# Kernel optimization log

Hardware: AMD Instinct MI355X
Metric: run time of the kernel (lower is better)

## Reference

```python
import jax, jax.numpy as jnp
import numpy as np

B, S, D, C = 8, 4096, 512, 2048


def setup_inputs() -> dict:
    key = jax.random.key(0)
    kx, kc = jax.random.split(key)
    x = jax.random.normal(kx, (B, S, D), dtype=jnp.float32)
    # kaiming_uniform_(a=sqrt(5)) on a [*,D,C] tensor ~ U(-bound, bound); exact init
    # distribution is irrelevant for the math, so plain scaled uniform is used.
    bound = 1.0 / np.sqrt(D)
    codebook = jax.random.uniform(kc, (1, 1, D, C), dtype=jnp.float32,
                                  minval=-bound, maxval=bound)
    return {"x": x, "codebook": codebook}


def reference(x, codebook):
    # Original: ((x[..., :, None] - codebook) ** 2).mean(dim=-2) -> [B, S, C]
    # Equivalent GEMM form: mean_d(x_d^2) + mean_d(c_dk^2) - (2/D) * x . c_k
    d = x.shape[-1]
    cb = codebook.reshape(codebook.shape[-2], codebook.shape[-1])  # [D, C]
    x2 = jnp.mean(x * x, axis=-1, keepdims=True)                   # [B, S, 1]
    c2 = jnp.mean(cb * cb, axis=0)                                 # [C]
    xc = jnp.einsum('bsd,dc->bsc', x, cb) / d                      # [B, S, C]
    return x2 + c2 - 2.0 * xc
```

## Files before the change

### kernel.cpp

```cpp
#include <hip/hip_runtime.h>
#include <hip/hip_bf16.h>


typedef __attribute__((ext_vector_type(8))) short bf16x8;
typedef __attribute__((ext_vector_type(4))) float f32x4;

#define M_ROWS 32768
#define K_DIM  512
#define N_COLS 2048

__device__ __forceinline__ unsigned short f2bf(float f) {
    unsigned int u = __float_as_uint(f);
    return (unsigned short)((u + 0x7fffu + ((u >> 16) & 1u)) >> 16);
}

__device__ __forceinline__ void gload_lds16(const void* g, void* l) {
    __builtin_amdgcn_global_load_lds(
        (const __attribute__((address_space(1))) unsigned int*)g,
        (__attribute__((address_space(3))) unsigned int*)l,
        16, 0, 0);
}

__global__ __launch_bounds__(256) void prep_x_kernel(const float* __restrict__ x,
                                                     unsigned short* __restrict__ xb,
                                                     float* __restrict__ x2) {
    const int wid = threadIdx.x >> 6;
    const int lane = threadIdx.x & 63;
    const int row = (blockIdx.x << 2) + wid;
    const float4* p4 = reinterpret_cast<const float4*>(x + (size_t)row * K_DIM);
    float4 v0 = p4[lane];
    float4 v1 = p4[lane + 64];
    float ss = v0.x*v0.x + v0.y*v0.y + v0.z*v0.z + v0.w*v0.w
             + v1.x*v1.x + v1.y*v1.y + v1.z*v1.z + v1.w*v1.w;
    union { unsigned short us[4]; uint2 u2; } pa, pb;
    pa.us[0] = f2bf(v0.x); pa.us[1] = f2bf(v0.y); pa.us[2] = f2bf(v0.z); pa.us[3] = f2bf(v0.w);
    pb.us[0] = f2bf(v1.x); pb.us[1] = f2bf(v1.y); pb.us[2] = f2bf(v1.z); pb.us[3] = f2bf(v1.w);
    uint2* dst = reinterpret_cast<uint2*>(xb + (size_t)row * K_DIM);
    dst[lane]      = pa.u2;
    dst[lane + 64] = pb.u2;
    #pragma unroll
    for (int off = 32; off; off >>= 1) ss += __shfl_xor(ss, off);
    if (lane == 0) x2[row] = ss * (1.0f / (float)K_DIM);
}

__global__ __launch_bounds__(256) void prep_cb_kernel(const float* __restrict__ cb,
                                                      unsigned short* __restrict__ cbT) {
    __shared__ float tile[32][65];
    const int k0 = blockIdx.x * 32;
    const int n0 = blockIdx.y * 64;
    const int tx = threadIdx.x & 63;
    const int ty = threadIdx.x >> 6;
    #pragma unroll
    for (int i = 0; i < 8; ++i) {
        const int k = ty + i * 4;
        tile[k][tx] = cb[(size_t)(k0 + k) * N_COLS + n0 + tx];
    }
    __syncthreads();
    const int kc = threadIdx.x & 31;
    const int nr = threadIdx.x >> 5;
    #pragma unroll
    for (int i = 0; i < 8; ++i) {
        const int n = nr + i * 8;
        cbT[(size_t)(n0 + n) * K_DIM + k0 + kc] = f2bf(tile[kc][n] * 0.00390625f);
    }
}

__global__ __launch_bounds__(256) void c2_kernel(const float* __restrict__ cb,
                                                 float* __restrict__ c2) {
    __shared__ float p[4][64];
    const int t = threadIdx.x;
    const int nl = t & 63;
    const int kc = t >> 6;
    const int n = blockIdx.x * 64 + nl;
    float s = 0.0f;
    for (int k = kc * 128; k < kc * 128 + 128; ++k) {
        float v = cb[(size_t)k * N_COLS + n];
        s += v * v;
    }
    p[kc][nl] = s;
    __syncthreads();
    if (t < 64) {
        c2[blockIdx.x * 64 + t] =
            (p[0][t] + p[1][t] + p[2][t] + p[3][t]) * (1.0f / (float)K_DIM);
    }
}

__global__ __launch_bounds__(256) void gemm_kernel(
        const unsigned short* __restrict__ A,
        const unsigned short* __restrict__ Bt,
        const float* __restrict__ x2,
        const float* __restrict__ c2,
        float* __restrict__ out) {
    __shared__ unsigned short As[128 * 32];
    __shared__ unsigned short Bs[128 * 32];
    const int tid  = threadIdx.x;
    const int wid  = tid >> 6;
    const int lane = tid & 63;
    const int wr = wid >> 1, wc = wid & 1;
    const int n0 = blockIdx.x * 128;
    const int m0 = blockIdx.y * 128;
    const int l15 = lane & 15;
    const int lhi = lane >> 4;

    f32x4 acc[4][4] = {};

    const unsigned short* Abase = A  + (size_t)m0 * K_DIM;
    const unsigned short* Bbase = Bt + (size_t)n0 * K_DIM;

    for (int k0 = 0; k0 < K_DIM; k0 += 32) {
        #pragma unroll
        for (int r = 0; r < 2; ++r) {
            const int ch  = r * 256 + tid;
            const int row = ch >> 2;
            const int ko  = (ch & 3) * 8;
            gload_lds16(Abase + (size_t)row * K_DIM + k0 + ko,
                        &As[(r * 256 + wid * 64) * 8]);
            gload_lds16(Bbase + (size_t)row * K_DIM + k0 + ko,
                        &Bs[(r * 256 + wid * 64) * 8]);
        }
        __syncthreads();

        bf16x8 aF[4], bF[4];
        #pragma unroll
        for (int i = 0; i < 4; ++i) {
            aF[i] = *reinterpret_cast<const bf16x8*>(&As[(wr * 64 + i * 16 + l15) * 32 + lhi * 8]);
            bF[i] = *reinterpret_cast<const bf16x8*>(&Bs[(wc * 64 + i * 16 + l15) * 32 + lhi * 8]);
        }
        #pragma unroll
        for (int i = 0; i < 4; ++i)
            #pragma unroll
            for (int j = 0; j < 4; ++j)
                acc[i][j] = __builtin_amdgcn_mfma_f32_16x16x32_bf16(aF[i], bF[j], acc[i][j], 0, 0, 0);
        __syncthreads();
    }

    #pragma unroll
    for (int i = 0; i < 4; ++i) {
        const int mrow = m0 + wr * 64 + i * 16 + lhi * 4;
        const float xv0 = x2[mrow + 0];
        const float xv1 = x2[mrow + 1];
        const float xv2 = x2[mrow + 2];
        const float xv3 = x2[mrow + 3];
        #pragma unroll
        for (int j = 0; j < 4; ++j) {
            const int n = n0 + wc * 64 + j * 16 + l15;
            const float cv = c2[n];
            float* o = out + (size_t)mrow * N_COLS + n;
            o[0 * N_COLS] = xv0 + cv - acc[i][j][0];
            o[1 * N_COLS] = xv1 + cv - acc[i][j][1];
            o[2 * N_COLS] = xv2 + cv - acc[i][j][2];
            o[3 * N_COLS] = xv3 + cv - acc[i][j][3];
        }
    }
}

extern "C" void kernel_launch(void* const* d_in, const int* in_sizes, int n_in,
                              void* d_out, int out_size, void* d_ws, size_t ws_size,
                              hipStream_t stream) {
    const float* x  = (const float*)d_in[0];
    const float* cb = (const float*)d_in[1];
    float* out = (float*)d_out;

    char* ws = (char*)d_ws;
    unsigned short* xb  = (unsigned short*)ws;
    unsigned short* cbT = (unsigned short*)(ws + (size_t)33554432);
    float* x2 = (float*)(ws + (size_t)33554432 + 2097152);
    float* c2 = (float*)(ws + (size_t)33554432 + 2097152 + 131072);

    prep_x_kernel<<<M_ROWS / 4, 256, 0, stream>>>(x, xb, x2);
    prep_cb_kernel<<<dim3(16, 32), 256, 0, stream>>>(cb, cbT);
    c2_kernel<<<N_COLS / 64, 256, 0, stream>>>(cb, c2);
    gemm_kernel<<<dim3(N_COLS / 128, M_ROWS / 128), 256, 0, stream>>>(xb, cbT, x2, c2, out);
}
```

Measured before the change: 151.9 us.

## Rewrite GEMM with 256x256 tiles, double-buffered swizzled LDS and XCD-aware block mapping

The GEMM now uses 512-thread blocks computing 256x256 output tiles with a K step of 64 split into half-tiles. Global-to-LDS loads are double-buffered and interleaved with MFMA phases using explicit vmcnt waits, raw barriers and s_setprio. LDS layout is XOR-swizzled to avoid bank conflicts, and the block index is remapped to group tiles per XCD for L2 reuse. This is meant to hide memory latency and raise MFMA utilization, at the cost of higher register and LDS pressure (128 KB LDS per block) and fragile manual synchronization.

Result: faster. 130.7 us (-13.9%).

```diff
diff --git a/kernel.cpp b/kernel.cpp
--- a/kernel.cpp
+++ b/kernel.cpp
@@ -8,6 +8,7 @@
 #define M_ROWS 32768
 #define K_DIM  512
 #define N_COLS 2048
+#define NT     8
 
 __device__ __forceinline__ unsigned short f2bf(float f) {
     unsigned int u = __float_as_uint(f);
@@ -85,71 +86,147 @@
     }
 }
 
-__global__ __launch_bounds__(256) void gemm_kernel(
+
+__device__ __forceinline__ void stage_half(const unsigned short* __restrict__ gbase,
+                                           unsigned short* lbase, int wid, int lane) {
+    #pragma unroll
+    for (int i = 0; i < 2; ++i) {
+        const int o16 = i * 512 + wid * 64 + lane;
+        const int row = o16 >> 2;
+        const int sl  = (o16 & 3) ^ ((row >> 1) & 3);
+        gload_lds16(gbase + (size_t)row * K_DIM + sl * 8,
+                    lbase + i * 4096 + wid * 512);
+    }
+}
+
+__device__ __forceinline__ bf16x8 frag_ld(const unsigned short* h, int r, int lhi) {
+    const int off = r * 32 + ((lhi ^ ((r >> 1) & 3)) << 3);
+    return *reinterpret_cast<const bf16x8*>(&h[off]);
+}
+
+#define BAR()  do { asm volatile("" ::: "memory"); \
+                    __builtin_amdgcn_s_barrier();  \
+                    asm volatile("" ::: "memory"); } while (0)
+
+__global__ __launch_bounds__(512, 2) void gemm_kernel(
         const unsigned short* __restrict__ A,
         const unsigned short* __restrict__ Bt,
         const float* __restrict__ x2,
         const float* __restrict__ c2,
         float* __restrict__ out) {
-    __shared__ unsigned short As[128 * 32];
-    __shared__ unsigned short Bs[128 * 32];
+    __shared__ unsigned short smem[2][4][256 * 32];
+
     const int tid  = threadIdx.x;
     const int wid  = tid >> 6;
     const int lane = tid & 63;
-    const int wr = wid >> 1, wc = wid & 1;
-    const int n0 = blockIdx.x * 128;
-    const int m0 = blockIdx.y * 128;
+    const int wr = wid >> 2;
+    const int wc = wid & 3;
     const int l15 = lane & 15;
     const int lhi = lane >> 4;
 
-    f32x4 acc[4][4] = {};
-
-    const unsigned short* Abase = A  + (size_t)m0 * K_DIM;
-    const unsigned short* Bbase = Bt + (size_t)n0 * K_DIM;
-
-    for (int k0 = 0; k0 < K_DIM; k0 += 32) {
-        #pragma unroll
-        for (int r = 0; r < 2; ++r) {
-            const int ch  = r * 256 + tid;
-            const int row = ch >> 2;
-            const int ko  = (ch & 3) * 8;
-            gload_lds16(Abase + (size_t)row * K_DIM + k0 + ko,
-                        &As[(r * 256 + wid * 64) * 8]);
-            gload_lds16(Bbase + (size_t)row * K_DIM + k0 + ko,
-                        &Bs[(r * 256 + wid * 64) * 8]);
-        }
-        __syncthreads();
-
-        bf16x8 aF[4], bF[4];
-        #pragma unroll
-        for (int i = 0; i < 4; ++i) {
-            aF[i] = *reinterpret_cast<const bf16x8*>(&As[(wr * 64 + i * 16 + l15) * 32 + lhi * 8]);
-            bF[i] = *reinterpret_cast<const bf16x8*>(&Bs[(wc * 64 + i * 16 + l15) * 32 + lhi * 8]);
-        }
-        #pragma unroll
-        for (int i = 0; i < 4; ++i)
-            #pragma unroll
-            for (int j = 0; j < 4; ++j)
-                acc[i][j] = __builtin_amdgcn_mfma_f32_16x16x32_bf16(aF[i], bF[j], acc[i][j], 0, 0, 0);
-        __syncthreads();
-    }
-
-    #pragma unroll
-    for (int i = 0; i < 4; ++i) {
-        const int mrow = m0 + wr * 64 + i * 16 + lhi * 4;
+    const int bid  = blockIdx.x;
+    const int lbid = (bid & 7) * 128 + (bid >> 3);
+    const int m0 = (lbid >> 3) * 256;
+    const int n0 = (lbid & 7) * 256;
+
+    const unsigned short* Ab = A  + (size_t)m0 * K_DIM;
+    const unsigned short* Bb = Bt + (size_t)n0 * K_DIM;
+
+    f32x4 acc[8][4] = {};
+
+    stage_half(Ab,      smem[0][0], wid, lane);
+    stage_half(Bb,      smem[0][2], wid, lane);
+    stage_half(Ab + 32, smem[0][1], wid, lane);
+    stage_half(Bb + 32, smem[0][3], wid, lane);
+    asm volatile("s_waitcnt vmcnt(4)" ::: "memory");
+    BAR();
+
+    for (int t = 0; t < NT; ++t) {
+        const int cur = t & 1, nxt = cur ^ 1;
+        const unsigned short* hA0 = smem[cur][0];
+        const unsigned short* hA1 = smem[cur][1];
+        const unsigned short* hB0 = smem[cur][2];
+        const unsigned short* hB1 = smem[cur][3];
+        const int kn = (t + 1) * 64;
+        const bool st = (t < NT - 1);
+        bf16x8 a[4], b[4];
+
+        if (st) stage_half(Ab + kn, smem[nxt][0], wid, lane);
+        #pragma unroll
+        for (int mf = 0; mf < 4; ++mf) a[mf] = frag_ld(hA0, wr * 128 + mf * 16 + l15, lhi);
+        #pragma unroll
+        for (int nf = 0; nf < 4; ++nf) b[nf] = frag_ld(hB0, wc * 64 + nf * 16 + l15, lhi);
+        BAR();
+        __builtin_amdgcn_s_setprio(1);
+        #pragma unroll
+        for (int mf = 0; mf < 4; ++mf)
+            #pragma unroll
+            for (int nf = 0; nf < 4; ++nf)
+                acc[mf][nf] = __builtin_amdgcn_mfma_f32_16x16x32_bf16(a[mf], b[nf], acc[mf][nf], 0, 0, 0);
+        __builtin_amdgcn_s_setprio(0);
+        BAR();
+
+        if (st) stage_half(Bb + kn, smem[nxt][2], wid, lane);
+        #pragma unroll
+        for (int mf = 0; mf < 4; ++mf) a[mf] = frag_ld(hA0, wr * 128 + (mf + 4) * 16 + l15, lhi);
+        BAR();
+        __builtin_amdgcn_s_setprio(1);
+        #pragma unroll
+        for (int mf = 0; mf < 4; ++mf)
+            #pragma unroll
+            for (int nf = 0; nf < 4; ++nf)
+                acc[mf + 4][nf] = __builtin_amdgcn_mfma_f32_16x16x32_bf16(a[mf], b[nf], acc[mf + 4][nf], 0, 0, 0);
+        __builtin_amdgcn_s_setprio(0);
+        if (st) asm volatile("s_waitcnt vmcnt(4)" ::: "memory");
+        else    asm volatile("s_waitcnt vmcnt(0)" ::: "memory");
+        BAR();
+
+        if (st) stage_half(Ab + kn + 32, smem[nxt][1], wid, lane);
+        #pragma unroll
+        for (int mf = 0; mf < 4; ++mf) a[mf] = frag_ld(hA1, wr * 128 + mf * 16 + l15, lhi);
+        #pragma unroll
+        for (int nf = 0; nf < 4; ++nf) b[nf] = frag_ld(hB1, wc * 64 + nf * 16 + l15, lhi);
+        BAR();
+        __builtin_amdgcn_s_setprio(1);
+        #pragma unroll
+        for (int mf = 0; mf < 4; ++mf)
+            #pragma unroll
+            for (int nf = 0; nf < 4; ++nf)
+                acc[mf][nf] = __builtin_amdgcn_mfma_f32_16x16x32_bf16(a[mf], b[nf], acc[mf][nf], 0, 0, 0);
+        __builtin_amdgcn_s_setprio(0);
+        BAR();
+
+        if (st) stage_half(Bb + kn + 32, smem[nxt][3], wid, lane);
+        #pragma unroll
+        for (int mf = 0; mf < 4; ++mf) a[mf] = frag_ld(hA1, wr * 128 + (mf + 4) * 16 + l15, lhi);
+        BAR();
+        __builtin_amdgcn_s_setprio(1);
+        #pragma unroll
+        for (int mf = 0; mf < 4; ++mf)
+            #pragma unroll
+            for (int nf = 0; nf < 4; ++nf)
+                acc[mf + 4][nf] = __builtin_amdgcn_mfma_f32_16x16x32_bf16(a[mf], b[nf], acc[mf + 4][nf], 0, 0, 0);
+        __builtin_amdgcn_s_setprio(0);
+        if (st) asm volatile("s_waitcnt vmcnt(4)" ::: "memory");
+        BAR();
+    }
+
+    #pragma unroll
+    for (int mf = 0; mf < 8; ++mf) {
+        const int mrow = m0 + wr * 128 + mf * 16 + lhi * 4;
         const float xv0 = x2[mrow + 0];
         const float xv1 = x2[mrow + 1];
         const float xv2 = x2[mrow + 2];
         const float xv3 = x2[mrow + 3];
         #pragma unroll
-        for (int j = 0; j < 4; ++j) {
-            const int n = n0 + wc * 64 + j * 16 + l15;
-            const float cv = c2[n];
-            float* o = out + (size_t)mrow * N_COLS + n;
-            o[0 * N_COLS] = xv0 + cv - acc[i][j][0];
-            o[1 * N_COLS] = xv1 + cv - acc[i][j][1];
-            o[2 * N_COLS] = xv2 + cv - acc[i][j][2];
-            o[3 * N_COLS] = xv3 + cv - acc[i][j][3];
+        for (int nf = 0; nf < 4; ++nf) {
+            const int col = n0 + wc * 64 + nf * 16 + l15;
+            const float cv = c2[col];
+            float* o = out + (size_t)mrow * N_COLS + col;
+            o[0 * N_COLS] = xv0 + cv - acc[mf][nf][0];
+            o[1 * N_COLS] = xv1 + cv - acc[mf][nf][1];
+            o[2 * N_COLS] = xv2 + cv - acc[mf][nf][2];
+            o[3 * N_COLS] = xv3 + cv - acc[mf][nf][3];
         }
     }
 }
@@ -170,5 +247,5 @@
     prep_x_kernel<<<M_ROWS / 4, 256, 0, stream>>>(x, xb, x2);
     prep_cb_kernel<<<dim3(16, 32), 256, 0, stream>>>(cb, cbT);
     c2_kernel<<<N_COLS / 64, 256, 0, stream>>>(cb, c2);
-    gemm_kernel<<<dim3(N_COLS / 128, M_ROWS / 128), 256, 0, stream>>>(xb, cbT, x2, c2, out);
-}
+    gemm_kernel<<<dim3((M_ROWS / 256) * (N_COLS / 256)), 512, 0, stream>>>(xb, cbT, x2, c2, out);
+}
```

## Rewrite GEMM as persistent double-buffered kernel overlapping epilogue stores with MFMA

Applied to the files above, without the earlier changes.

The GEMM becomes a persistent kernel with 256 blocks of 512 threads. Each block owns 256 rows and sweeps 8 column tiles of 128 over half of N. Shared-memory tiles are double-buffered and XOR-swizzled, and loads are gated with explicit vmcnt waits and barriers. The previous tile's accumulators are stored while the current tile's MFMAs run, which hides output write traffic behind compute. The cost is complex hand-scheduled macros, a risk of races in the waitcnt gating, and higher register pressure from two accumulator sets.

After: 207.3 us. 1.36x slower.

```diff
diff --git a/kernel.cpp b/kernel.cpp
--- a/kernel.cpp
+++ b/kernel.cpp
@@ -85,73 +85,197 @@
     }
 }
 
-__global__ __launch_bounds__(256) void gemm_kernel(
+#define A0OFF 0
+#define A1OFF 8192
+#define B0OFF 16384
+#define B1OFF 20480
+
+__device__ __forceinline__ void stage_halfA(const unsigned short* __restrict__ g,
+                                            unsigned short* l, int wid, int lane) {
+    #pragma unroll
+    for (int i = 0; i < 2; ++i) {
+        const int o16 = i * 512 + wid * 64 + lane;
+        const int row = o16 >> 2;
+        const int sl  = (o16 & 3) ^ ((row >> 1) & 3);
+        gload_lds16(g + (size_t)row * K_DIM + sl * 8, l + i * 4096 + wid * 512);
+    }
+}
+__device__ __forceinline__ void stage_halfB(const unsigned short* __restrict__ g,
+                                            unsigned short* l, int wid, int lane) {
+    const int o16 = wid * 64 + lane;
+    const int row = o16 >> 2;
+    const int sl  = (o16 & 3) ^ ((row >> 1) & 3);
+    gload_lds16(g + (size_t)row * K_DIM + sl * 8, l + wid * 512);
+}
+
+__device__ __forceinline__ bf16x8 frag_ld(const unsigned short* h, int r, int lhi) {
+    const int off = r * 32 + ((lhi ^ ((r >> 1) & 3)) << 3);
+    return *reinterpret_cast<const bf16x8*>(&h[off]);
+}
+
+#define BAR()  do { asm volatile("" ::: "memory"); \
+                    __builtin_amdgcn_s_barrier();  \
+                    asm volatile("" ::: "memory"); } while (0)
+#define GATE_(n) asm volatile("s_waitcnt vmcnt(" #n ")" ::: "memory")
+#define GATE(n) GATE_(n)
+
+#define STORE1(OACC, IDX)                                                      \
+  { const int i_ = (IDX);                                                      \
+    const int mf_ = i_ >> 4, nf_ = (i_ >> 2) & 3, jj_ = i_ & 3;                \
+    outOld[(size_t)(mf_ * 16 + jj_) * N_COLS + nf_ * 16] =                     \
+        x2v[mf_ * 4 + jj_] + c2o[nf_] - OACC[mf_][nf_][jj_]; }
+
+#define MFMA8(ACCC, BASE)                                                      \
+  _Pragma("unroll")                                                            \
+  for (int nf_ = 0; nf_ < 4; ++nf_) {                                          \
+    ACCC[(BASE)][nf_]     = __builtin_amdgcn_mfma_f32_16x16x32_bf16(a[(BASE)],     b[nf_], ACCC[(BASE)][nf_],     0, 0, 0); \
+    ACCC[(BASE) + 1][nf_] = __builtin_amdgcn_mfma_f32_16x16x32_bf16(a[(BASE) + 1], b[nf_], ACCC[(BASE) + 1][nf_], 0, 0, 0); \
+  }
+
+#define KTILE(KT, ACCC, ACCO, DOST, G1N, G2N, DOG2, GA, GB, DOSTG)             \
+  {                                                                            \
+    const unsigned short* hA0_ = &smem[(KT) & 1][A0OFF];                       \
+    const unsigned short* hA1_ = &smem[(KT) & 1][A1OFF];                       \
+    const unsigned short* hB0_ = &smem[(KT) & 1][B0OFF];                       \
+    const unsigned short* hB1_ = &smem[(KT) & 1][B1OFF];                       \
+    unsigned short* nxt_ = smem[((KT) + 1) & 1];                               \
+                                                                  \
+    if (DOSTG) stage_halfA(GA, nxt_ + A0OFF, wid, lane);                       \
+    a[0] = frag_ld(hA0_, wr64 +  0 + l15, lhi);                                \
+    a[1] = frag_ld(hA0_, wr64 + 16 + l15, lhi);                                \
+    _Pragma("unroll")                                                          \
+    for (int nf_ = 0; nf_ < 4; ++nf_)                                          \
+        b[nf_] = frag_ld(hB0_, wc64 + nf_ * 16 + l15, lhi);                    \
+    BAR();                                                                     \
+    __builtin_amdgcn_s_setprio(1);                                             \
+    MFMA8(ACCC, 0);                                                            \
+    __builtin_amdgcn_s_setprio(0);                                             \
+    if (DOST) { STORE1(ACCO, (KT) * 8 + 0); STORE1(ACCO, (KT) * 8 + 1); }      \
+    BAR();                                                                     \
+                                                                  \
+    if (DOSTG) stage_halfB(GB, nxt_ + B0OFF, wid, lane);                       \
+    a[2] = frag_ld(hA0_, wr64 + 32 + l15, lhi);                                \
+    a[3] = frag_ld(hA0_, wr64 + 48 + l15, lhi);                                \
+    BAR();                                                                     \
+    __builtin_amdgcn_s_setprio(1);                                             \
+    MFMA8(ACCC, 2);                                                            \
+    __builtin_amdgcn_s_setprio(0);                                             \
+    if (DOST) { STORE1(ACCO, (KT) * 8 + 2); STORE1(ACCO, (KT) * 8 + 3); }      \
+    GATE(G1N);                                                                 \
+    BAR();                                                                     \
+                                                                  \
+    if (DOSTG) stage_halfA(GA + 32, nxt_ + A1OFF, wid, lane);                  \
+    a[0] = frag_ld(hA1_, wr64 +  0 + l15, lhi);                                \
+    a[1] = frag_ld(hA1_, wr64 + 16 + l15, lhi);                                \
+    _Pragma("unroll")                                                          \
+    for (int nf_ = 0; nf_ < 4; ++nf_)                                          \
+        b[nf_] = frag_ld(hB1_, wc64 + nf_ * 16 + l15, lhi);                    \
+    BAR();                                                                     \
+    __builtin_amdgcn_s_setprio(1);                                             \
+    MFMA8(ACCC, 0);                                                            \
+    __builtin_amdgcn_s_setprio(0);                                             \
+    if (DOST) { STORE1(ACCO, (KT) * 8 + 4); STORE1(ACCO, (KT) * 8 + 5); }      \
+    BAR();                                                                     \
+                                                                  \
+    if (DOSTG) stage_halfB(GB + 32, nxt_ + B1OFF, wid, lane);                  \
+    a[2] = frag_ld(hA1_, wr64 + 32 + l15, lhi);                                \
+    a[3] = frag_ld(hA1_, wr64 + 48 + l15, lhi);                                \
+    BAR();                                                                     \
+    __builtin_amdgcn_s_setprio(1);                                             \
+    MFMA8(ACCC, 2);                                                            \
+    __builtin_amdgcn_s_setprio(0);                                             \
+    if (DOST) { STORE1(ACCO, (KT) * 8 + 6); STORE1(ACCO, (KT) * 8 + 7); }      \
+    if (DOG2) { GATE(G2N); }                                                   \
+    BAR();                                                                     \
+  }
+
+#define TILE8(ACCC, ACCO, DOST, G1K0, G1M, G2M, BCUR, GB7, KT7G1, KT7DOG2, KT7STG) \
+  KTILE(0, ACCC, ACCO, DOST, G1K0,  G2M, 1, Ab +  64, (BCUR) +  64, 1)         \
+  KTILE(1, ACCC, ACCO, DOST, G1M,   G2M, 1, Ab + 128, (BCUR) + 128, 1)         \
+  KTILE(2, ACCC, ACCO, DOST, G1M,   G2M, 1, Ab + 192, (BCUR) + 192, 1)         \
+  KTILE(3, ACCC, ACCO, DOST, G1M,   G2M, 1, Ab + 256, (BCUR) + 256, 1)         \
+  KTILE(4, ACCC, ACCO, DOST, G1M,   G2M, 1, Ab + 320, (BCUR) + 320, 1)         \
+  KTILE(5, ACCC, ACCO, DOST, G1M,   G2M, 1, Ab + 384, (BCUR) + 384, 1)         \
+  KTILE(6, ACCC, ACCO, DOST, G1M,   G2M, 1, Ab + 448, (BCUR) + 448, 1)         \
+  KTILE(7, ACCC, ACCO, DOST, KT7G1, G2M, KT7DOG2, Ab, (GB7), KT7STG)
+
+#define ZERO_ACC(A_)                                                           \
+  _Pragma("unroll")                                                            \
+  for (int z_ = 0; z_ < 4; ++z_)                                               \
+    _Pragma("unroll")                                                          \
+    for (int w_ = 0; w_ < 4; ++w_)                                             \
+      A_[z_][w_] = (f32x4){0.f, 0.f, 0.f, 0.f};
+
+#define PREP_OLD(JOLD)                                                         \
+  { const int nold_ = nbase + (JOLD) * 128 + wc64 + l15;                       \
+    _Pragma("unroll")                                                          \
+    for (int q_ = 0; q_ < 4; ++q_) c2o[q_] = c2[nold_ + q_ * 16];              \
+    outOld = out + (size_t)(m0 + wr64 + lhi * 4) * N_COLS + nold_; }
+
+__global__ __launch_bounds__(512, 2) void gemm_kernel(
         const unsigned short* __restrict__ A,
         const unsigned short* __restrict__ Bt,
         const float* __restrict__ x2,
         const float* __restrict__ c2,
         float* __restrict__ out) {
-    __shared__ unsigned short As[128 * 32];
-    __shared__ unsigned short Bs[128 * 32];
+    __shared__ unsigned short smem[2][24576];
+
     const int tid  = threadIdx.x;
     const int wid  = tid >> 6;
     const int lane = tid & 63;
-    const int wr = wid >> 1, wc = wid & 1;
-    const int n0 = blockIdx.x * 128;
-    const int m0 = blockIdx.y * 128;
+    const int wr64 = (wid >> 1) * 64;
+    const int wc64 = (wid & 1) * 64;
     const int l15 = lane & 15;
     const int lhi = lane >> 4;
 
-    f32x4 acc[4][4] = {};
-
-    const unsigned short* Abase = A  + (size_t)m0 * K_DIM;
-    const unsigned short* Bbase = Bt + (size_t)n0 * K_DIM;
-
-    for (int k0 = 0; k0 < K_DIM; k0 += 32) {
+    const int bid  = blockIdx.x;
+    const int lbid = (bid & 7) * 32 + (bid >> 3);
+    const int m0    = (lbid >> 1) * 256;
+    const int nbase = (lbid & 1) * 1024;
+
+    const unsigned short* Ab = A + (size_t)m0 * K_DIM;
+
+    f32x4 accA[4][4] = {};
+    f32x4 accB[4][4] = {};
+    bf16x8 a[4], b[4];
+    float c2o[4];
+    float* outOld = nullptr;
+
+    float x2v[16];
+    #pragma unroll
+    for (int mf = 0; mf < 4; ++mf)
         #pragma unroll
-        for (int r = 0; r < 2; ++r) {
-            const int ch  = r * 256 + tid;
-            const int row = ch >> 2;
-            const int ko  = (ch & 3) * 8;
-            gload_lds16(Abase + (size_t)row * K_DIM + k0 + ko,
-                        &As[(r * 256 + wid * 64) * 8]);
-            gload_lds16(Bbase + (size_t)row * K_DIM + k0 + ko,
-                        &Bs[(r * 256 + wid * 64) * 8]);
-        }
-        __syncthreads();
-
-        bf16x8 aF[4], bF[4];
-        #pragma unroll
-        for (int i = 0; i < 4; ++i) {
-            aF[i] = *reinterpret_cast<const bf16x8*>(&As[(wr * 64 + i * 16 + l15) * 32 + lhi * 8]);
-            bF[i] = *reinterpret_cast<const bf16x8*>(&Bs[(wc * 64 + i * 16 + l15) * 32 + lhi * 8]);
-        }
-        #pragma unroll
-        for (int i = 0; i < 4; ++i)
-            #pragma unroll
-            for (int j = 0; j < 4; ++j)
-                acc[i][j] = __builtin_amdgcn_mfma_f32_16x16x32_bf16(aF[i], bF[j], acc[i][j], 0, 0, 0);
-        __syncthreads();
-    }
-
-    #pragma unroll
-    for (int i = 0; i < 4; ++i) {
-        const int mrow = m0 + wr * 64 + i * 16 + lhi * 4;
-        const float xv0 = x2[mrow + 0];
-        const float xv1 = x2[mrow + 1];
-        const float xv2 = x2[mrow + 2];
-        const float xv3 = x2[mrow + 3];
-        #pragma unroll
-        for (int j = 0; j < 4; ++j) {
-            const int n = n0 + wc * 64 + j * 16 + l15;
-            const float cv = c2[n];
-            float* o = out + (size_t)mrow * N_COLS + n;
-            o[0 * N_COLS] = xv0 + cv - acc[i][j][0];
-            o[1 * N_COLS] = xv1 + cv - acc[i][j][1];
-            o[2 * N_COLS] = xv2 + cv - acc[i][j][2];
-            o[3 * N_COLS] = xv3 + cv - acc[i][j][3];
-        }
-    }
+        for (int jj = 0; jj < 4; ++jj)
+            x2v[mf * 4 + jj] = x2[m0 + wr64 + mf * 16 + lhi * 4 + jj];
+
+    const unsigned short* B0p = Bt + (size_t)nbase * K_DIM;
+    stage_halfA(Ab,      smem[0] + A0OFF, wid, lane);
+    stage_halfB(B0p,     smem[0] + B0OFF, wid, lane);
+    stage_halfA(Ab + 32, smem[0] + A1OFF, wid, lane);
+    stage_halfB(B0p + 32, smem[0] + B1OFF, wid, lane);
+    GATE(3);
+    BAR();
+
+    TILE8(accA, accB, 0, 3, 3, 3, B0p, B0p + 128 * (size_t)K_DIM, 3, 1, 1);
+
+    const unsigned short* Bcur = B0p + 128 * (size_t)K_DIM;
+    for (int p = 0; p < 3; ++p) {
+        PREP_OLD(2 * p);
+        ZERO_ACC(accB);
+        TILE8(accB, accA, 1, 7, 9, 9, Bcur, Bcur + 128 * (size_t)K_DIM, 9, 1, 1);
+        Bcur += 128 * (size_t)K_DIM;
+        PREP_OLD(2 * p + 1);
+        ZERO_ACC(accA);
+        TILE8(accA, accB, 1, 7, 9, 9, Bcur, Bcur + 128 * (size_t)K_DIM, 9, 1, 1);
+        Bcur += 128 * (size_t)K_DIM;
+    }
+    PREP_OLD(6);
+    ZERO_ACC(accB);
+    TILE8(accB, accA, 1, 7, 9, 9, Bcur, Ab , 6, 0, 0);
+
+    PREP_OLD(7);
+    #pragma unroll
+    for (int i = 0; i < 64; ++i) { STORE1(accB, i); }
 }
 
 extern "C" void kernel_launch(void* const* d_in, const int* in_sizes, int n_in,
@@ -170,5 +294,5 @@
     prep_x_kernel<<<M_ROWS / 4, 256, 0, stream>>>(x, xb, x2);
     prep_cb_kernel<<<dim3(16, 32), 256, 0, stream>>>(cb, cbT);
     c2_kernel<<<N_COLS / 64, 256, 0, stream>>>(cb, c2);
-    gemm_kernel<<<dim3(N_COLS / 128, M_ROWS / 128), 256, 0, stream>>>(xb, cbT, x2, c2, out);
-}
+    gemm_kernel<<<256, 512, 0, stream>>>(xb, cbT, x2, c2, out);
+}
```

## Triple-buffer GEMM K-loop with async LDS loads, swizzle, and 128x256 tiles

Applied to the files above, without the earlier changes.

The GEMM moves to 512-thread blocks computing 128x256 output tiles. A three-stage LDS ring is filled by direct global-to-LDS loads two K-steps ahead, gated with explicit vmcnt waits and a single barrier per step instead of two syncthreads. LDS rows are XOR-swizzled to reduce bank conflicts on fragment reads, and block IDs are remapped so neighbouring blocks share tiles in cache. MFMA sections also get raised wave priority. The cost is more LDS per block and tighter hand-managed synchronisation.

Measured after the change: 122.7 us. -19.2%, faster.

```diff
diff --git a/kernel.cpp b/kernel.cpp
--- a/kernel.cpp
+++ b/kernel.cpp
@@ -85,71 +85,106 @@
     }
 }
 
-__global__ __launch_bounds__(256) void gemm_kernel(
+
+__device__ __forceinline__ bf16x8 frag_ld(const unsigned short* h, int r, int lhi) {
+    const int off = r * 32 + ((lhi ^ ((r >> 1) & 3)) << 3);
+    return *reinterpret_cast<const bf16x8*>(&h[off]);
+}
+
+#define BAR()  do { asm volatile("" ::: "memory"); \
+                    __builtin_amdgcn_s_barrier();  \
+                    asm volatile("" ::: "memory"); } while (0)
+#define GATE_(n) asm volatile("s_waitcnt vmcnt(" #n ")" ::: "memory")
+#define GATE(n) GATE_(n)
+
+__global__ __launch_bounds__(512, 4) void gemm_kernel(
         const unsigned short* __restrict__ A,
         const unsigned short* __restrict__ Bt,
         const float* __restrict__ x2,
         const float* __restrict__ c2,
         float* __restrict__ out) {
-    __shared__ unsigned short As[128 * 32];
-    __shared__ unsigned short Bs[128 * 32];
+    __shared__ unsigned short smem[3][12288];
+
     const int tid  = threadIdx.x;
     const int wid  = tid >> 6;
     const int lane = tid & 63;
-    const int wr = wid >> 1, wc = wid & 1;
-    const int n0 = blockIdx.x * 128;
-    const int m0 = blockIdx.y * 128;
+    const int wr64 = (wid >> 2) * 64;
+    const int wc64 = (wid & 3) * 64;
     const int l15 = lane & 15;
     const int lhi = lane >> 4;
 
+    const int bid  = blockIdx.x;
+    const int lbid = (bid & 7) * 256 + (bid >> 3);
+    const int m0 = (lbid >> 3) * 128;
+    const int n0 = (lbid & 7) * 256;
+
+    const unsigned short* Ab = A  + (size_t)m0 * K_DIM;
+    const unsigned short* Bb = Bt + (size_t)n0 * K_DIM;
+
+    const int o16a  = wid * 64 + lane;
+    const int rowa  = o16a >> 2;
+    const int sla   = (o16a & 3) ^ ((rowa >> 1) & 3);
+    const size_t aoff = (size_t)rowa * K_DIM + sla * 8;
+    const int o16b0 = wid * 64 + lane;
+    const int rowb0 = o16b0 >> 2;
+    const size_t boff0 = (size_t)rowb0 * K_DIM + (((o16b0 & 3) ^ ((rowb0 >> 1) & 3)) * 8);
+    const int o16b1 = 512 + wid * 64 + lane;
+    const int rowb1 = o16b1 >> 2;
+    const size_t boff1 = (size_t)rowb1 * K_DIM + (((o16b1 & 3) ^ ((rowb1 >> 1) & 3)) * 8);
+
     f32x4 acc[4][4] = {};
 
-    const unsigned short* Abase = A  + (size_t)m0 * K_DIM;
-    const unsigned short* Bbase = Bt + (size_t)n0 * K_DIM;
-
-    for (int k0 = 0; k0 < K_DIM; k0 += 32) {
-        #pragma unroll
-        for (int r = 0; r < 2; ++r) {
-            const int ch  = r * 256 + tid;
-            const int row = ch >> 2;
-            const int ko  = (ch & 3) * 8;
-            gload_lds16(Abase + (size_t)row * K_DIM + k0 + ko,
-                        &As[(r * 256 + wid * 64) * 8]);
-            gload_lds16(Bbase + (size_t)row * K_DIM + k0 + ko,
-                        &Bs[(r * 256 + wid * 64) * 8]);
-        }
-        __syncthreads();
-
-        bf16x8 aF[4], bF[4];
-        #pragma unroll
-        for (int i = 0; i < 4; ++i) {
-            aF[i] = *reinterpret_cast<const bf16x8*>(&As[(wr * 64 + i * 16 + l15) * 32 + lhi * 8]);
-            bF[i] = *reinterpret_cast<const bf16x8*>(&Bs[(wc * 64 + i * 16 + l15) * 32 + lhi * 8]);
-        }
-        #pragma unroll
-        for (int i = 0; i < 4; ++i)
+#define STAGE(KT, BUF)                                                         \
+    do {                                                                       \
+        gload_lds16(Ab + aoff  + (KT) * 32, &smem[(BUF)][wid * 512]);          \
+        gload_lds16(Bb + boff0 + (KT) * 32, &smem[(BUF)][4096 + wid * 512]);   \
+        gload_lds16(Bb + boff1 + (KT) * 32, &smem[(BUF)][8192 + wid * 512]);   \
+    } while (0)
+
+    STAGE(0, 0);
+    STAGE(1, 1);
+    GATE(3);
+    BAR();
+
+    #pragma unroll
+    for (int t = 0; t < 16; ++t) {
+        if (t < 14) STAGE(t + 2, (t + 2) % 3);
+        const unsigned short* cbuf = smem[t % 3];
+        bf16x8 a[4], b[4];
+        #pragma unroll
+        for (int mf = 0; mf < 4; ++mf)
+            a[mf] = frag_ld(cbuf, wr64 + mf * 16 + l15, lhi);
+        #pragma unroll
+        for (int nf = 0; nf < 4; ++nf)
+            b[nf] = frag_ld(cbuf + 4096, wc64 + nf * 16 + l15, lhi);
+        __builtin_amdgcn_s_setprio(1);
+        #pragma unroll
+        for (int mf = 0; mf < 4; ++mf)
             #pragma unroll
-            for (int j = 0; j < 4; ++j)
-                acc[i][j] = __builtin_amdgcn_mfma_f32_16x16x32_bf16(aF[i], bF[j], acc[i][j], 0, 0, 0);
-        __syncthreads();
-    }
-
-    #pragma unroll
-    for (int i = 0; i < 4; ++i) {
-        const int mrow = m0 + wr * 64 + i * 16 + lhi * 4;
+            for (int nf = 0; nf < 4; ++nf)
+                acc[mf][nf] = __builtin_amdgcn_mfma_f32_16x16x32_bf16(a[mf], b[nf], acc[mf][nf], 0, 0, 0);
+        __builtin_amdgcn_s_setprio(0);
+        if (t < 14) { GATE(3); } else if (t == 14) { GATE(0); }
+        BAR();
+    }
+#undef STAGE
+
+    #pragma unroll
+    for (int mf = 0; mf < 4; ++mf) {
+        const int mrow = m0 + wr64 + mf * 16 + lhi * 4;
         const float xv0 = x2[mrow + 0];
         const float xv1 = x2[mrow + 1];
         const float xv2 = x2[mrow + 2];
         const float xv3 = x2[mrow + 3];
         #pragma unroll
-        for (int j = 0; j < 4; ++j) {
-            const int n = n0 + wc * 64 + j * 16 + l15;
-            const float cv = c2[n];
-            float* o = out + (size_t)mrow * N_COLS + n;
-            o[0 * N_COLS] = xv0 + cv - acc[i][j][0];
-            o[1 * N_COLS] = xv1 + cv - acc[i][j][1];
-            o[2 * N_COLS] = xv2 + cv - acc[i][j][2];
-            o[3 * N_COLS] = xv3 + cv - acc[i][j][3];
+        for (int nf = 0; nf < 4; ++nf) {
+            const int col = n0 + wc64 + nf * 16 + l15;
+            const float cv = c2[col];
+            float* o = out + (size_t)mrow * N_COLS + col;
+            o[0 * N_COLS] = xv0 + cv - acc[mf][nf][0];
+            o[1 * N_COLS] = xv1 + cv - acc[mf][nf][1];
+            o[2 * N_COLS] = xv2 + cv - acc[mf][nf][2];
+            o[3 * N_COLS] = xv3 + cv - acc[mf][nf][3];
         }
     }
 }
@@ -170,5 +205,5 @@
     prep_x_kernel<<<M_ROWS / 4, 256, 0, stream>>>(x, xb, x2);
     prep_cb_kernel<<<dim3(16, 32), 256, 0, stream>>>(cb, cbT);
     c2_kernel<<<N_COLS / 64, 256, 0, stream>>>(cb, c2);
-    gemm_kernel<<<dim3(N_COLS / 128, M_ROWS / 128), 256, 0, stream>>>(xb, cbT, x2, c2, out);
-}
+    gemm_kernel<<<dim3((M_ROWS / 128) * (N_COLS / 256)), 512, 0, stream>>>(xb, cbT, x2, c2, out);
+}
```
